# Performance work log

Measured on AMD Instinct MI355X. Metric: run time of the kernel, lower is better.

The kernel has to match this reference:

```python
import jax, jax.numpy as jnp
import numpy as np


def _v2v_mean(X, pair_v, pair_e, num_edges):
    """Hypergraph v2v mean aggregation: vertex->edge mean, then edge->vertex mean.
    X: [N, C] vertex features; (pair_v, pair_e): incidence pairs."""
    num_v = X.shape[0]
    ones = jnp.ones((pair_v.shape[0],), X.dtype)
    # v2e mean: average member-vertex features per hyperedge
    e_sum = jax.ops.segment_sum(X[pair_v], pair_e, num_segments=num_edges)
    e_cnt = jax.ops.segment_sum(ones, pair_e, num_segments=num_edges)
    Xe = e_sum / jnp.maximum(e_cnt, 1.0)[:, None]  # [E, C]
    # e2v mean: average incident-hyperedge features per vertex
    v_sum = jax.ops.segment_sum(Xe[pair_e], pair_v, num_segments=num_v)
    v_cnt = jax.ops.segment_sum(ones, pair_v, num_segments=num_v)
    return v_sum / jnp.maximum(v_cnt, 1.0)[:, None]  # [N, C]


def setup_inputs() -> dict:
    key = jax.random.key(0)
    ks = jax.random.split(key, 6)
    N, E, P = 16384, 2048, 262144          # vertices, hyperedges, incidence pairs
    Cin, Ch, Cout = 1024, 1024, 512
    feature_hyg = jax.random.normal(ks[0], (N, Cin), jnp.float32)
    pair_v = jax.random.randint(ks[1], (P,), 0, N)
    pair_e = jax.random.randint(ks[2], (P,), 0, E)
    W1 = jax.random.normal(ks[3], (Cin, Ch), jnp.float32) / np.float32(np.sqrt(Cin))
    b1 = jnp.zeros((Ch,), jnp.float32)
    W2 = jax.random.normal(ks[4], (Ch, Cout), jnp.float32) / np.float32(np.sqrt(Ch))
    b2 = jnp.zeros((Cout,), jnp.float32)
    return {"feature_hyg": feature_hyg, "pair_v": pair_v, "pair_e": pair_e,
            "num_edges": E, "W1": W1, "b1": b1, "W2": W2, "b2": b2}


def reference(feature_hyg, pair_v, pair_e, num_edges, W1, b1, W2, b2):
    # HGNNPConv layer 1 (use_bn=False, drop_rate=0.0, eval-mode dropout)
    X = jax.nn.relu(feature_hyg @ W1 + b1)   # theta + relu
    X = _v2v_mean(X, pair_v, pair_e, num_edges)
    X = jax.nn.relu(X)                       # self.act (dropout is identity)
    # HGNNPConv layer 2 (is_last=True)
    X = jax.nn.relu(X @ W2 + b2)
    X = _v2v_mean(X, pair_v, pair_e, num_edges)
    return X
```

## Files before the change

### kernel.cpp

```cpp
#include <hip/hip_runtime.h>

typedef __attribute__((ext_vector_type(8))) short short8;
typedef __attribute__((ext_vector_type(4))) float f32x4;

constexpr int Nv   = 16384;
constexpr int Ne   = 2048;
constexpr int Np   = 262144;
constexpr int Cin  = 1024;
constexpr int Chid = 1024;
constexpr int Cout = 512;

__device__ __forceinline__ ushort f2bf(float f){
  unsigned u = __float_as_uint(f);
  u += 0x7FFFu + ((u >> 16) & 1u);
  return (ushort)(u >> 16);
}
__device__ __forceinline__ float bf2f(ushort h){
  return __uint_as_float(((unsigned)h) << 16);
}


__global__ void count_pairs(const int* __restrict__ pv, const int* __restrict__ pe,
                            int* __restrict__ vcnt, int* __restrict__ ecnt){
  int p = blockIdx.x * blockDim.x + threadIdx.x;
  if (p < Np){
    atomicAdd(&ecnt[pe[p]], 1);
    atomicAdd(&vcnt[pv[p]], 1);
  }
}

__global__ void scan_excl(const int* __restrict__ cnt, int* __restrict__ off, int n){
  __shared__ int s[1024];
  __shared__ int carry_s;
  if (threadIdx.x == 0) carry_s = 0;
  __syncthreads();
  for (int base = 0; base < n; base += 1024){
    int i = base + (int)threadIdx.x;
    int v = (i < n) ? cnt[i] : 0;
    s[threadIdx.x] = v;
    __syncthreads();
    for (int d = 1; d < 1024; d <<= 1){
      int t = (threadIdx.x >= (unsigned)d) ? s[threadIdx.x - d] : 0;
      __syncthreads();
      s[threadIdx.x] += t;
      __syncthreads();
    }
    int incl = s[threadIdx.x];
    int carry = carry_s;
    if (i < n) off[i] = carry + incl - v;
    __syncthreads();
    if (threadIdx.x == 1023) carry_s = carry + s[1023];
    __syncthreads();
  }
  if (threadIdx.x == 0) off[n] = carry_s;
}

__global__ void fill_adj(const int* __restrict__ pv, const int* __restrict__ pe,
                         const int* __restrict__ eoff, int* __restrict__ efill, int* __restrict__ eadj,
                         const int* __restrict__ voff, int* __restrict__ vfill, int* __restrict__ vadj){
  int p = blockIdx.x * blockDim.x + threadIdx.x;
  if (p < Np){
    int e = pe[p], v = pv[p];
    int ie = atomicAdd(&efill[e], 1);
    eadj[eoff[e] + ie] = v;
    int iv = atomicAdd(&vfill[v], 1);
    vadj[voff[v] + iv] = e;
  }
}


__global__ void cvt_f32_bf16(const float* __restrict__ in, ushort* __restrict__ out, int n4){
  int i = blockIdx.x * blockDim.x + threadIdx.x;
  if (i < n4){
    float4 f = ((const float4*)in)[i];
    ushort4 o;
    o.x = f2bf(f.x); o.y = f2bf(f.y); o.z = f2bf(f.z); o.w = f2bf(f.w);
    ((ushort4*)out)[i] = o;
  }
}

__global__ void transpose_cvt(const float* __restrict__ in, ushort* __restrict__ out,
                              int R, int Ccols){
  __shared__ float t[32][33];
  int c0 = blockIdx.x * 32, r0 = blockIdx.y * 32;
  int tx = threadIdx.x, ty = threadIdx.y;
  for (int j = 0; j < 32; j += 8)
    t[ty + j][tx] = in[(size_t)(r0 + ty + j) * Ccols + (c0 + tx)];
  __syncthreads();
  for (int j = 0; j < 32; j += 8)
    out[(size_t)(c0 + ty + j) * R + (r0 + tx)] = f2bf(t[tx][ty + j]);
}


template<bool BIAS_RELU, bool OUT_BF16>
__global__ __launch_bounds__(256) void gemm_bt(
    const ushort* __restrict__ A, const ushort* __restrict__ BT,
    const float* __restrict__ bias, void* __restrict__ out,
    int M, int Nn, int K)
{
  __shared__ ushort As[128][40];
  __shared__ ushort Bs[128][40];
  const int tid  = threadIdx.x;
  const int lane = tid & 63;
  const int wave = tid >> 6;
  const int wm = wave >> 1, wn = wave & 1;
  const int m0 = blockIdx.x * 128, n0 = blockIdx.y * 128;

  f32x4 acc[4][4] = {};

  const int r  = tid >> 1;
  const int c0 = (tid & 1) * 16;
  const int fr = lane & 15;
  const int kb = (lane >> 4) * 8;

  for (int k0 = 0; k0 < K; k0 += 32){
    __syncthreads();
    const ushort* pa = &A [(size_t)(m0 + r) * K + k0 + c0];
    const ushort* pb = &BT[(size_t)(n0 + r) * K + k0 + c0];
    short8 a0 = *(const short8*)pa;
    short8 a1 = *(const short8*)(pa + 8);
    short8 b0 = *(const short8*)pb;
    short8 b1 = *(const short8*)(pb + 8);
    *(short8*)&As[r][c0]     = a0;
    *(short8*)&As[r][c0 + 8] = a1;
    *(short8*)&Bs[r][c0]     = b0;
    *(short8*)&Bs[r][c0 + 8] = b1;
    __syncthreads();

    short8 af[4], bfv[4];
#pragma unroll
    for (int m = 0; m < 4; ++m) af[m]  = *(const short8*)&As[wm * 64 + m * 16 + fr][kb];
#pragma unroll
    for (int n = 0; n < 4; ++n) bfv[n] = *(const short8*)&Bs[wn * 64 + n * 16 + fr][kb];
#pragma unroll
    for (int m = 0; m < 4; ++m)
#pragma unroll
      for (int n = 0; n < 4; ++n)
        acc[m][n] = __builtin_amdgcn_mfma_f32_16x16x32_bf16(af[m], bfv[n], acc[m][n], 0, 0, 0);
  }

#pragma unroll
  for (int m = 0; m < 4; ++m){
#pragma unroll
    for (int n = 0; n < 4; ++n){
      int row0 = m0 + wm * 64 + m * 16 + ((lane >> 4) * 4);
      int col  = n0 + wn * 64 + n * 16 + (lane & 15);
      float bv = BIAS_RELU ? bias[col] : 0.0f;
#pragma unroll
      for (int i = 0; i < 4; ++i){
        int row = row0 + i;
        float v = acc[m][n][i];
        if (BIAS_RELU){ v += bv; v = v > 0.0f ? v : 0.0f; }
        if (OUT_BF16) ((ushort*)out)[(size_t)row * Nn + col] = f2bf(v);
        else          ((float*) out)[(size_t)row * Nn + col] = v;
      }
    }
  }
}


template<int C, bool OUTF32>
__global__ void v2e_mean(const ushort* __restrict__ Xin, const int* __restrict__ eoff,
                         const int* __restrict__ eadj, void* __restrict__ out){
  __shared__ int vs[256];
  const int e = blockIdx.x;
  const int tid = threadIdx.x;
  const int c = tid * 4;
  const int beg = eoff[e], end = eoff[e + 1];
  float a0 = 0.f, a1 = 0.f, a2 = 0.f, a3 = 0.f;
  for (int base = beg; base < end; base += blockDim.x){
    int nchunk = min((int)blockDim.x, end - base);
    __syncthreads();
    if (tid < nchunk) vs[tid] = eadj[base + tid];
    __syncthreads();
    for (int j = 0; j < nchunk; ++j){
      int v = vs[j];
      ushort4 x = *(const ushort4*)&Xin[(size_t)v * C + c];
      a0 += bf2f(x.x); a1 += bf2f(x.y); a2 += bf2f(x.z); a3 += bf2f(x.w);
    }
  }
  float inv = 1.0f / (float)max(end - beg, 1);
  a0 *= inv; a1 *= inv; a2 *= inv; a3 *= inv;
  if (OUTF32){
    float4 o = {a0, a1, a2, a3};
    *(float4*)&((float*)out)[(size_t)e * C + c] = o;
  } else {
    ushort4 o = {f2bf(a0), f2bf(a1), f2bf(a2), f2bf(a3)};
    *(ushort4*)&((ushort*)out)[(size_t)e * C + c] = o;
  }
}

template<int C, bool BIASRELU, bool OUTBF16>
__global__ void e2v_mean(const float* __restrict__ Ein, const int* __restrict__ voff,
                         const int* __restrict__ vadj, const float* __restrict__ bias,
                         void* __restrict__ out){
  __shared__ int es[128];
  const int v = blockIdx.x;
  const int tid = threadIdx.x;
  const int c = tid * 4;
  const int beg = voff[v], end = voff[v + 1];
  float a0 = 0.f, a1 = 0.f, a2 = 0.f, a3 = 0.f;
  for (int base = beg; base < end; base += blockDim.x){
    int nchunk = min((int)blockDim.x, end - base);
    __syncthreads();
    if (tid < nchunk) es[tid] = vadj[base + tid];
    __syncthreads();
    for (int j = 0; j < nchunk; ++j){
      int e = es[j];
      float4 z = *(const float4*)&Ein[(size_t)e * C + c];
      a0 += z.x; a1 += z.y; a2 += z.z; a3 += z.w;
    }
  }
  float inv = 1.0f / (float)max(end - beg, 1);
  a0 *= inv; a1 *= inv; a2 *= inv; a3 *= inv;
  if (BIASRELU){
    a0 += bias[c];     a1 += bias[c + 1]; a2 += bias[c + 2]; a3 += bias[c + 3];
    a0 = a0 > 0.f ? a0 : 0.f;  a1 = a1 > 0.f ? a1 : 0.f;
    a2 = a2 > 0.f ? a2 : 0.f;  a3 = a3 > 0.f ? a3 : 0.f;
  }
  if (OUTBF16){
    ushort4 o = {f2bf(a0), f2bf(a1), f2bf(a2), f2bf(a3)};
    *(ushort4*)&((ushort*)out)[(size_t)v * C + c] = o;
  } else {
    float4 o = {a0, a1, a2, a3};
    *(float4*)&((float*)out)[(size_t)v * C + c] = o;
  }
}


extern "C" void kernel_launch(void* const* d_in, const int* in_sizes, int n_in,
                              void* d_out, int out_size, void* d_ws, size_t ws_size,
                              hipStream_t stream){
  (void)in_sizes; (void)n_in; (void)out_size; (void)ws_size;
  const float* feat = (const float*)d_in[0];
  const int*   pv   = (const int*)d_in[1];
  const int*   pe   = (const int*)d_in[2];
  const float* W1   = (const float*)d_in[4];
  const float* b1   = (const float*)d_in[5];
  const float* W2   = (const float*)d_in[6];
  const float* b2   = (const float*)d_in[7];

  char* ws = (char*)d_ws;
  size_t off = 0;
  auto alloc = [&](size_t bytes) -> void* {
    void* p = ws + off;
    off += (bytes + 255) & ~(size_t)255;
    return p;
  };

  ushort* X1bf = (ushort*)alloc((size_t)Nv * Chid * 2);
  ushort* Xe1  = (ushort*)alloc((size_t)Ne * Chid * 2);
  float*  Ze   = (float*) alloc((size_t)Ne * Cout * 4);
  char*  regA  = (char*)  alloc((size_t)Nv * Cin  * 2);
  ushort* Abf  = (ushort*)regA;
  ushort* X3bf = (ushort*)regA;
  float*  Xe2  = (float*)(regA + (size_t)Nv * Cout * 2);
  ushort* W1T  = (ushort*)alloc((size_t)Chid * Cin * 2);
  ushort* W2T  = (ushort*)alloc((size_t)Cout * Chid * 2);

  int* zr     = (int*)alloc((size_t)(Ne + Nv + Ne + Nv) * 4);
  int* e_cnt  = zr;
  int* v_cnt  = zr + Ne;
  int* e_fill = zr + Ne + Nv;
  int* v_fill = zr + Ne + Nv + Ne;
  int* e_off  = (int*)alloc((size_t)(Ne + 1) * 4);
  int* v_off  = (int*)alloc((size_t)(Nv + 1) * 4);
  int* e_adj  = (int*)alloc((size_t)Np * 4);
  int* v_adj  = (int*)alloc((size_t)Np * 4);

  hipMemsetAsync(zr, 0, (size_t)(Ne + Nv + Ne + Nv) * 4, stream);
  count_pairs<<<(Np + 255) / 256, 256, 0, stream>>>(pv, pe, v_cnt, e_cnt);
  scan_excl<<<1, 1024, 0, stream>>>(e_cnt, e_off, Ne);
  scan_excl<<<1, 1024, 0, stream>>>(v_cnt, v_off, Nv);
  fill_adj<<<(Np + 255) / 256, 256, 0, stream>>>(pv, pe, e_off, e_fill, e_adj,
                                                 v_off, v_fill, v_adj);

  cvt_f32_bf16<<<(Nv * Cin / 4 + 255) / 256, 256, 0, stream>>>(feat, Abf, Nv * Cin / 4);
  transpose_cvt<<<dim3(Chid / 32, Cin / 32), dim3(32, 8), 0, stream>>>(W1, W1T, Cin, Chid);
  transpose_cvt<<<dim3(Cout / 32, Chid / 32), dim3(32, 8), 0, stream>>>(W2, W2T, Chid, Cout);

  gemm_bt<true, true><<<dim3(Nv / 128, Chid / 128), 256, 0, stream>>>(
      Abf, W1T, b1, X1bf, Nv, Chid, Cin);

  v2e_mean<Chid, false><<<Ne, Chid / 4, 0, stream>>>(X1bf, e_off, e_adj, Xe1);

  gemm_bt<false, false><<<dim3(Ne / 128, Cout / 128), 256, 0, stream>>>(
      Xe1, W2T, nullptr, Ze, Ne, Cout, Chid);

  e2v_mean<Cout, true, true><<<Nv, Cout / 4, 0, stream>>>(Ze, v_off, v_adj, b2, X3bf);

  v2e_mean<Cout, true><<<Ne, Cout / 4, 0, stream>>>(X3bf, e_off, e_adj, Xe2);
  e2v_mean<Cout, false, false><<<Nv, Cout / 4, 0, stream>>>(Xe2, v_off, v_adj, nullptr, (float*)d_out);
}
```

Measured before the change: 493.7 us.

## Apply W2 before hypergraph aggregation and narrow gathers to 512 bf16 columns

Reorders layer 2 so the linear W2 projection runs on all vertex features before the v2e mean, relying on linearity of the mean. Every aggregation then gathers 512-wide bf16 rows instead of 1024-wide rows, and the edge intermediates are stored in bf16 instead of f32, which cuts gather traffic. The cost is a GEMM that runs over 16384 rows instead of 2048, so it does about 8x more FLOPs. The GEMM also stages tiles with global_load_lds into unpadded LDS, which may introduce bank conflicts, and the scan now uses wave shuffles.

```diff
diff --git a/kernel.cpp b/kernel.cpp
--- a/kernel.cpp
+++ b/kernel.cpp
@@ -19,6 +19,12 @@
   return __uint_as_float(((unsigned)h) << 16);
 }
 
+__device__ __forceinline__ void gload16(const void* g, void* lds){
+  __builtin_amdgcn_global_load_lds(
+      (const __attribute__((address_space(1))) void*)g,
+      (__attribute__((address_space(3))) void*)lds, 16, 0, 0);
+}
+
 
 __global__ void count_pairs(const int* __restrict__ pv, const int* __restrict__ pe,
                             int* __restrict__ vcnt, int* __restrict__ ecnt){
@@ -30,26 +36,29 @@
 }
 
 __global__ void scan_excl(const int* __restrict__ cnt, int* __restrict__ off, int n){
-  __shared__ int s[1024];
+  __shared__ int wsum[16];
   __shared__ int carry_s;
+  const int lane = threadIdx.x & 63, wid = threadIdx.x >> 6;
   if (threadIdx.x == 0) carry_s = 0;
   __syncthreads();
   for (int base = 0; base < n; base += 1024){
     int i = base + (int)threadIdx.x;
     int v = (i < n) ? cnt[i] : 0;
-    s[threadIdx.x] = v;
-    __syncthreads();
-    for (int d = 1; d < 1024; d <<= 1){
-      int t = (threadIdx.x >= (unsigned)d) ? s[threadIdx.x - d] : 0;
-      __syncthreads();
-      s[threadIdx.x] += t;
-      __syncthreads();
+    int s = v;
+#pragma unroll
+    for (int d = 1; d < 64; d <<= 1){
+      int t = __shfl_up(s, d, 64);
+      if (lane >= d) s += t;
     }
-    int incl = s[threadIdx.x];
+    if (lane == 63) wsum[wid] = s;
+    __syncthreads();
+    int wadd = 0;
+#pragma unroll
+    for (int w = 0; w < 16; ++w) if (w < wid) wadd += wsum[w];
     int carry = carry_s;
-    if (i < n) off[i] = carry + incl - v;
-    __syncthreads();
-    if (threadIdx.x == 1023) carry_s = carry + s[1023];
+    if (i < n) off[i] = carry + wadd + s - v;
+    __syncthreads();
+    if (threadIdx.x == 1023) carry_s = carry + wadd + s;
     __syncthreads();
   }
   if (threadIdx.x == 0) off[n] = carry_s;
@@ -98,8 +107,8 @@
     const float* __restrict__ bias, void* __restrict__ out,
     int M, int Nn, int K)
 {
-  __shared__ ushort As[128][40];
-  __shared__ ushort Bs[128][40];
+  __shared__ ushort As[128 * 32];
+  __shared__ ushort Bs[128 * 32];
   const int tid  = threadIdx.x;
   const int lane = tid & 63;
   const int wave = tid >> 6;
@@ -108,30 +117,34 @@
 
   f32x4 acc[4][4] = {};
 
-  const int r  = tid >> 1;
-  const int c0 = (tid & 1) * 16;
+  const int srow = tid >> 2;
+  const int scol = (tid & 3) * 8;
+  ushort* ldsA0 = &As[(wave * 16) * 32];
+  ushort* ldsA1 = &As[(64 + wave * 16) * 32];
+  ushort* ldsB0 = &Bs[(wave * 16) * 32];
+  ushort* ldsB1 = &Bs[(64 + wave * 16) * 32];
+
   const int fr = lane & 15;
   const int kb = (lane >> 4) * 8;
 
+  const size_t arow0 = (size_t)(m0 + srow) * K;
+  const size_t arow1 = (size_t)(m0 + 64 + srow) * K;
+  const size_t brow0 = (size_t)(n0 + srow) * K;
+  const size_t brow1 = (size_t)(n0 + 64 + srow) * K;
+
   for (int k0 = 0; k0 < K; k0 += 32){
     __syncthreads();
-    const ushort* pa = &A [(size_t)(m0 + r) * K + k0 + c0];
-    const ushort* pb = &BT[(size_t)(n0 + r) * K + k0 + c0];
-    short8 a0 = *(const short8*)pa;
-    short8 a1 = *(const short8*)(pa + 8);
-    short8 b0 = *(const short8*)pb;
-    short8 b1 = *(const short8*)(pb + 8);
-    *(short8*)&As[r][c0]     = a0;
-    *(short8*)&As[r][c0 + 8] = a1;
-    *(short8*)&Bs[r][c0]     = b0;
-    *(short8*)&Bs[r][c0 + 8] = b1;
+    gload16(A  + arow0 + k0 + scol, ldsA0);
+    gload16(A  + arow1 + k0 + scol, ldsA1);
+    gload16(BT + brow0 + k0 + scol, ldsB0);
+    gload16(BT + brow1 + k0 + scol, ldsB1);
     __syncthreads();
 
     short8 af[4], bfv[4];
 #pragma unroll
-    for (int m = 0; m < 4; ++m) af[m]  = *(const short8*)&As[wm * 64 + m * 16 + fr][kb];
-#pragma unroll
-    for (int n = 0; n < 4; ++n) bfv[n] = *(const short8*)&Bs[wn * 64 + n * 16 + fr][kb];
+    for (int m = 0; m < 4; ++m) af[m]  = *(const short8*)&As[(wm * 64 + m * 16 + fr) * 32 + kb];
+#pragma unroll
+    for (int n = 0; n < 4; ++n) bfv[n] = *(const short8*)&Bs[(wn * 64 + n * 16 + fr) * 32 + kb];
 #pragma unroll
     for (int m = 0; m < 4; ++m)
 #pragma unroll
@@ -159,71 +172,40 @@
 }
 
 
-template<int C, bool OUTF32>
-__global__ void v2e_mean(const ushort* __restrict__ Xin, const int* __restrict__ eoff,
-                         const int* __restrict__ eadj, void* __restrict__ out){
-  __shared__ int vs[256];
-  const int e = blockIdx.x;
+template<bool BIASRELU, bool OUTBF16>
+__global__ void seg_mean512(const ushort* __restrict__ Xin, const int* __restrict__ off,
+                            const int* __restrict__ adj, const float* __restrict__ bias,
+                            void* __restrict__ out){
+  __shared__ int idx[128];
+  const int s = blockIdx.x;
   const int tid = threadIdx.x;
   const int c = tid * 4;
-  const int beg = eoff[e], end = eoff[e + 1];
+  const int beg = off[s], end = off[s + 1];
   float a0 = 0.f, a1 = 0.f, a2 = 0.f, a3 = 0.f;
-  for (int base = beg; base < end; base += blockDim.x){
-    int nchunk = min((int)blockDim.x, end - base);
-    __syncthreads();
-    if (tid < nchunk) vs[tid] = eadj[base + tid];
-    __syncthreads();
-    for (int j = 0; j < nchunk; ++j){
-      int v = vs[j];
-      ushort4 x = *(const ushort4*)&Xin[(size_t)v * C + c];
+  for (int base = beg; base < end; base += 128){
+    int nch = min(128, end - base);
+    __syncthreads();
+    if (tid < nch) idx[tid] = adj[base + tid];
+    __syncthreads();
+#pragma unroll 4
+    for (int j = 0; j < nch; ++j){
+      const ushort4 x = *(const ushort4*)&Xin[(size_t)idx[j] * 512 + c];
       a0 += bf2f(x.x); a1 += bf2f(x.y); a2 += bf2f(x.z); a3 += bf2f(x.w);
-    }
-  }
-  float inv = 1.0f / (float)max(end - beg, 1);
-  a0 *= inv; a1 *= inv; a2 *= inv; a3 *= inv;
-  if (OUTF32){
-    float4 o = {a0, a1, a2, a3};
-    *(float4*)&((float*)out)[(size_t)e * C + c] = o;
-  } else {
-    ushort4 o = {f2bf(a0), f2bf(a1), f2bf(a2), f2bf(a3)};
-    *(ushort4*)&((ushort*)out)[(size_t)e * C + c] = o;
-  }
-}
-
-template<int C, bool BIASRELU, bool OUTBF16>
-__global__ void e2v_mean(const float* __restrict__ Ein, const int* __restrict__ voff,
-                         const int* __restrict__ vadj, const float* __restrict__ bias,
-                         void* __restrict__ out){
-  __shared__ int es[128];
-  const int v = blockIdx.x;
-  const int tid = threadIdx.x;
-  const int c = tid * 4;
-  const int beg = voff[v], end = voff[v + 1];
-  float a0 = 0.f, a1 = 0.f, a2 = 0.f, a3 = 0.f;
-  for (int base = beg; base < end; base += blockDim.x){
-    int nchunk = min((int)blockDim.x, end - base);
-    __syncthreads();
-    if (tid < nchunk) es[tid] = vadj[base + tid];
-    __syncthreads();
-    for (int j = 0; j < nchunk; ++j){
-      int e = es[j];
-      float4 z = *(const float4*)&Ein[(size_t)e * C + c];
-      a0 += z.x; a1 += z.y; a2 += z.z; a3 += z.w;
     }
   }
   float inv = 1.0f / (float)max(end - beg, 1);
   a0 *= inv; a1 *= inv; a2 *= inv; a3 *= inv;
   if (BIASRELU){
-    a0 += bias[c];     a1 += bias[c + 1]; a2 += bias[c + 2]; a3 += bias[c + 3];
-    a0 = a0 > 0.f ? a0 : 0.f;  a1 = a1 > 0.f ? a1 : 0.f;
-    a2 = a2 > 0.f ? a2 : 0.f;  a3 = a3 > 0.f ? a3 : 0.f;
+    const float4 b = *(const float4*)&bias[c];
+    a0 = fmaxf(a0 + b.x, 0.f); a1 = fmaxf(a1 + b.y, 0.f);
+    a2 = fmaxf(a2 + b.z, 0.f); a3 = fmaxf(a3 + b.w, 0.f);
   }
   if (OUTBF16){
     ushort4 o = {f2bf(a0), f2bf(a1), f2bf(a2), f2bf(a3)};
-    *(ushort4*)&((ushort*)out)[(size_t)v * C + c] = o;
+    *(ushort4*)&((ushort*)out)[(size_t)s * 512 + c] = o;
   } else {
     float4 o = {a0, a1, a2, a3};
-    *(float4*)&((float*)out)[(size_t)v * C + c] = o;
+    *(float4*)&((float*)out)[(size_t)s * 512 + c] = o;
   }
 }
 
@@ -248,13 +230,13 @@
     return p;
   };
 
+  char* buf0 = (char*)alloc((size_t)Nv * Cin * 2);
+  ushort* Abf = (ushort*)buf0;
+  ushort* Y1  = (ushort*)buf0;
+  ushort* X3  = (ushort*)(buf0 + (size_t)Nv * Cout * 2);
   ushort* X1bf = (ushort*)alloc((size_t)Nv * Chid * 2);
-  ushort* Xe1  = (ushort*)alloc((size_t)Ne * Chid * 2);
-  float*  Ze   = (float*) alloc((size_t)Ne * Cout * 4);
-  char*  regA  = (char*)  alloc((size_t)Nv * Cin  * 2);
-  ushort* Abf  = (ushort*)regA;
-  ushort* X3bf = (ushort*)regA;
-  float*  Xe2  = (float*)(regA + (size_t)Nv * Cout * 2);
+  ushort* Ze   = (ushort*)alloc((size_t)Ne * Cout * 2);
+  ushort* Xe2  = (ushort*)alloc((size_t)Ne * Cout * 2);
   ushort* W1T  = (ushort*)alloc((size_t)Chid * Cin * 2);
   ushort* W2T  = (ushort*)alloc((size_t)Cout * Chid * 2);
 
@@ -282,13 +264,13 @@
   gemm_bt<true, true><<<dim3(Nv / 128, Chid / 128), 256, 0, stream>>>(
       Abf, W1T, b1, X1bf, Nv, Chid, Cin);
 
-  v2e_mean<Chid, false><<<Ne, Chid / 4, 0, stream>>>(X1bf, e_off, e_adj, Xe1);
-
-  gemm_bt<false, false><<<dim3(Ne / 128, Cout / 128), 256, 0, stream>>>(
-      Xe1, W2T, nullptr, Ze, Ne, Cout, Chid);
-
-  e2v_mean<Cout, true, true><<<Nv, Cout / 4, 0, stream>>>(Ze, v_off, v_adj, b2, X3bf);
-
-  v2e_mean<Cout, true><<<Ne, Cout / 4, 0, stream>>>(X3bf, e_off, e_adj, Xe2);
-  e2v_mean<Cout, false, false><<<Nv, Cout / 4, 0, stream>>>(Xe2, v_off, v_adj, nullptr, (float*)d_out);
-}
+  gemm_bt<false, true><<<dim3(Nv / 128, Cout / 128), 256, 0, stream>>>(
+      X1bf, W2T, nullptr, Y1, Nv, Cout, Chid);
+
+  seg_mean512<false, true><<<Ne, 128, 0, stream>>>(Y1, e_off, e_adj, nullptr, Ze);
+
+  seg_mean512<true, true><<<Nv, 128, 0, stream>>>(Ze, v_off, v_adj, b2, X3);
+
+  seg_mean512<false, true><<<Ne, 128, 0, stream>>>(X3, e_off, e_adj, nullptr, Xe2);
+  seg_mean512<false, false><<<Nv, 128, 0, stream>>>(Xe2, v_off, v_adj, nullptr, (float*)d_out);
+}
```

Result: faster. 420.6 us (-14.8%).
